# Kernel optimization log

Hardware: AMD Instinct MI355X
Metric: run time of the kernel (lower is better)

Reference implementation:

```python
import jax, jax.numpy as jnp
import numpy as np

B, C, H, W = 8, 64, 64, 64
MID = C // 8  # = 8, single-head key/query dim


def setup_inputs() -> dict:
    key = jax.random.key(0)
    ks = jax.random.split(key, 8)
    return {
        "x": jax.random.normal(ks[0], (B, C, H, W), dtype=jnp.float32),
        "wq": jax.random.normal(ks[1], (MID, C), dtype=jnp.float32) * 0.1,
        "bq": jax.random.normal(ks[2], (MID,), dtype=jnp.float32) * 0.1,
        "wk": jax.random.normal(ks[3], (MID, C), dtype=jnp.float32) * 0.1,
        "bk": jax.random.normal(ks[4], (MID,), dtype=jnp.float32) * 0.1,
        "wv": jax.random.normal(ks[5], (C, C), dtype=jnp.float32) * 0.1,
        "bv": jax.random.normal(ks[6], (C,), dtype=jnp.float32) * 0.1,
        "gamma": jax.random.uniform(ks[7], (1,), dtype=jnp.float32),
    }


def reference(x, wq, bq, wk, bk, wv, bv, gamma):
    b, c, h, w = x.shape
    n = h * w
    xf = x.reshape(b, c, n)  # [B, C, N]
    # 1x1 convs == per-pixel linear projections
    q = jnp.einsum("mc,bcn->bmn", wq, xf) + bq[:, None]  # [B, MID, N]
    k = jnp.einsum("mc,bcn->bmn", wk, xf) + bk[:, None]  # [B, MID, N]
    v = jnp.einsum("dc,bcn->bdn", wv, xf) + bv[:, None]  # [B, C, N]
    # attn[b, i, j] = softmax_j( q[:, i] . k[:, j] )  -- no scaling (SAGAN)
    attn = jax.nn.softmax(jnp.einsum("bmi,bmj->bij", q, k), axis=-1)  # [B, N, N]
    # out[b, c, i] = sum_j v[b, c, j] * attn[b, i, j]
    out = jnp.einsum("bcj,bij->bci", v, attn).reshape(b, c, h, w)
    return x + gamma[0] * out
```

## Files before the change

### kernel.cpp

```cpp
#include <hip/hip_runtime.h>
#include <math.h>

#define NB 8
#define NC 64
#define NN 4096
#define PS 72
#define LOG2E 1.4426950408889634f

typedef __attribute__((ext_vector_type(8))) short short8;
typedef __attribute__((ext_vector_type(4))) float float4v;

#if __has_builtin(__builtin_amdgcn_exp2f)
#define EXP2F(v) __builtin_amdgcn_exp2f(v)
#else
#define EXP2F(v) __expf((v) * 0.6931471805599453f)
#endif

__device__ inline unsigned short f2bf(float f) {
    unsigned int u = __builtin_bit_cast(unsigned int, f);
    unsigned int r = (u + 0x7FFFu + ((u >> 16) & 1u)) >> 16;
    return (unsigned short)r;
}
__device__ inline unsigned int bfpack(float lo, float hi) {
    unsigned int a = __builtin_bit_cast(unsigned int, lo) + 0x8000u;
    unsigned int b = __builtin_bit_cast(unsigned int, hi) + 0x8000u;
    return __builtin_amdgcn_perm(b, a, 0x07060302u);
}

__global__ __launch_bounds__(256) void prepack_kernel(
    const float* __restrict__ wq, const float* __restrict__ bq,
    const float* __restrict__ wk, const float* __restrict__ bk,
    const float* __restrict__ wv, const float* __restrict__ bv,
    unsigned short* __restrict__ wpack, float* __restrict__ bpack)
{
    const int tid = threadIdx.x;
    for (int item = tid; item < 640; item += 256) {
        const int f = item >> 6, lane = item & 63;
        const int mt = f >> 1, kc = f & 1;
        const int c0 = lane & 15, quad = lane >> 4;
        const float* row;
        float scale = 1.f;
        if (mt < 4) row = wv + (mt * 16 + c0) * 64;
        else if (c0 < 8) { row = wq + c0 * 64; scale = LOG2E; }
        else row = wk + (c0 - 8) * 64;
        unsigned short* dst = wpack + ((size_t)f * 64 + lane) * 8;
        for (int e = 0; e < 8; ++e) dst[e] = f2bf(row[kc * 32 + quad * 8 + e] * scale);
    }
    if (tid < 80) {
        float v;
        if (tid < 64) v = bv[tid];
        else if (tid < 72) v = bq[tid - 64] * LOG2E;
        else v = bk[tid - 72];
        bpack[tid] = v;
    }
}

__global__ __launch_bounds__(64) void proj_mfma_kernel(
    const float* __restrict__ x,
    const unsigned short* __restrict__ wpack, const float* __restrict__ bpack,
    unsigned short* __restrict__ qo8, unsigned short* __restrict__ ko8,
    unsigned short* __restrict__ vo)
{
    const int b = blockIdx.y;
    const int lane = threadIdx.x;
    const int c0 = lane & 15, quad = lane >> 4;
    const int n0 = blockIdx.x * 16;

    __shared__ unsigned short qkb[16][24];

    short8 wf[10];
#pragma unroll
    for (int f = 0; f < 10; ++f)
        wf[f] = *(const short8*)(wpack + ((size_t)f * 64 + lane) * 8);

    const float* xb = x + (size_t)b * NC * NN + n0 + c0;
    short8 xf[2];
#pragma unroll
    for (int kc = 0; kc < 2; ++kc)
#pragma unroll
        for (int e = 0; e < 8; ++e)
            xf[kc][e] = (short)f2bf(xb[(size_t)(kc * 32 + quad * 8 + e) * NN]);

#pragma unroll
    for (int mt = 0; mt < 4; ++mt) {
        float4v acc = {0.f, 0.f, 0.f, 0.f};
        acc = __builtin_amdgcn_mfma_f32_16x16x32_bf16(wf[mt * 2], xf[0], acc, 0, 0, 0);
        acc = __builtin_amdgcn_mfma_f32_16x16x32_bf16(wf[mt * 2 + 1], xf[1], acc, 0, 0, 0);
#pragma unroll
        for (int reg = 0; reg < 4; ++reg) {
            int ch = mt * 16 + quad * 4 + reg;
            vo[((size_t)b * NC + ch) * NN + n0 + c0] = f2bf(acc[reg] + bpack[ch]);
        }
    }

    {
        float4v acc = {0.f, 0.f, 0.f, 0.f};
        acc = __builtin_amdgcn_mfma_f32_16x16x32_bf16(wf[8], xf[0], acc, 0, 0, 0);
        acc = __builtin_amdgcn_mfma_f32_16x16x32_bf16(wf[9], xf[1], acc, 0, 0, 0);
        float a[4];
#pragma unroll
        for (int reg = 0; reg < 4; ++reg)
            a[reg] = acc[reg] + bpack[64 + quad * 4 + reg];
        *(uint2*)&qkb[c0][quad * 4] = make_uint2(bfpack(a[0], a[1]), bfpack(a[2], a[3]));
        if (quad == 0) {
            uint4 qrow = *(const uint4*)&qkb[c0][0];
            uint4 krow = *(const uint4*)&qkb[c0][8];
            *(uint4*)&qo8[((size_t)b * NN + n0 + c0) * 8] = qrow;
            *(uint4*)&ko8[((size_t)b * NN + n0 + c0) * 8] = krow;
        }
    }
}

__global__ __launch_bounds__(256, 4) void attn_fused_kernel(
    const unsigned short* __restrict__ qo8, const unsigned short* __restrict__ ko8,
    const unsigned short* __restrict__ vo,
    const float* __restrict__ x, const float* __restrict__ gamma,
    float* __restrict__ out)
{
    const int b = blockIdx.x;
    const int i0b = blockIdx.y * 32;
    const int wave = threadIdx.x >> 6, lane = threadIdx.x & 63;
    const int c0 = lane & 15, quad = lane >> 4;

    __shared__ __align__(16) float obuf[4][32][65];
    __shared__ float lbuf[4][2][16];

    unsigned short* psw = (unsigned short*)obuf + wave * 16 * PS;
    unsigned short* pswr = psw + c0 * PS + quad * 4;
    const unsigned short* psrd = psw + c0 * PS + quad * 8;

    const int jbase = wave * (NN / 4);

    short8 qf[2] = {};
    if (quad == 0) {
        qf[0] = *(const short8*)(qo8 + ((size_t)b * NN + i0b + c0) * 8);
        qf[1] = *(const short8*)(qo8 + ((size_t)b * NN + i0b + 16 + c0) * 8);
    } else if (quad == 1) {
        qf[0][0] = (short)0xC1E7;
        qf[1][0] = (short)0xC1E7;
    }

    float4v acc[2][4];
#pragma unroll
    for (int qh = 0; qh < 2; ++qh)
#pragma unroll
        for (int ct = 0; ct < 4; ++ct) acc[qh][ct] = (float4v){0.f, 0.f, 0.f, 0.f};
    float lsum[2] = {0.f, 0.f};

    const unsigned short* vbase = vo + ((size_t)b * NC + c0) * NN + jbase + quad * 8;
    const unsigned short* kbase = ko8 + ((size_t)(b * NN + jbase + c0)) * 8;

    short8 vc0[4];
#pragma unroll
    for (int ct = 0; ct < 4; ++ct)
        vc0[ct] = *(const short8*)(vbase + (size_t)ct * 16 * NN);

    for (int t = 0; t < NN / 4 / 64; ++t) {
        const int jt = t * 64;
        short8 kf[4] = {};
        if (quad == 0) {
#pragma unroll
            for (int st = 0; st < 4; ++st)
                kf[st] = *(const short8*)(kbase + (size_t)(jt + st * 16) * 8);
        } else if (quad == 1) {
            kf[0][0] = (short)0x3F80; kf[1][0] = (short)0x3F80;
            kf[2][0] = (short)0x3F80; kf[3][0] = (short)0x3F80;
        }
        short8 vc1[4], vn0[4];
#pragma unroll
        for (int ct = 0; ct < 4; ++ct)
            vc1[ct] = *(const short8*)(vbase + (size_t)ct * 16 * NN + jt + 32);
        if (t < NN / 4 / 64 - 1) {
#pragma unroll
            for (int ct = 0; ct < 4; ++ct)
                vn0[ct] = *(const short8*)(vbase + (size_t)ct * 16 * NN + jt + 64);
        }

#pragma unroll
        for (int qh = 0; qh < 2; ++qh) {
            float4v s[4];
#pragma unroll
            for (int st = 0; st < 4; ++st) {
                float4v z = {0.f, 0.f, 0.f, 0.f};
                s[st] = __builtin_amdgcn_mfma_f32_16x16x32_bf16(kf[st], qf[qh], z, 0, 0, 0);
            }
#pragma unroll
            for (int st = 0; st < 4; ++st) {
                float p0 = EXP2F(s[st][0]);
                float p1 = EXP2F(s[st][1]);
                float p2 = EXP2F(s[st][2]);
                float p3 = EXP2F(s[st][3]);
                lsum[qh] += (p0 + p1) + (p2 + p3);
                *(uint2*)(pswr + st * 16) = make_uint2(bfpack(p0, p1), bfpack(p2, p3));
            }
            {
                short8 pf0 = *(const short8*)(psrd);
#pragma unroll
                for (int ct = 0; ct < 4; ++ct)
                    acc[qh][ct] = __builtin_amdgcn_mfma_f32_16x16x32_bf16(
                        pf0, vc0[ct], acc[qh][ct], 0, 0, 0);
                short8 pf1 = *(const short8*)(psrd + 32);
#pragma unroll
                for (int ct = 0; ct < 4; ++ct)
                    acc[qh][ct] = __builtin_amdgcn_mfma_f32_16x16x32_bf16(
                        pf1, vc1[ct], acc[qh][ct], 0, 0, 0);
            }
        }
#pragma unroll
        for (int ct = 0; ct < 4; ++ct) vc0[ct] = vn0[ct];
    }

#pragma unroll
    for (int qh = 0; qh < 2; ++qh) {
        lsum[qh] += __shfl_xor(lsum[qh], 16);
        lsum[qh] += __shfl_xor(lsum[qh], 32);
    }

    __syncthreads();

    if (quad == 0) {
        lbuf[wave][0][c0] = lsum[0];
        lbuf[wave][1][c0] = lsum[1];
    }
#pragma unroll
    for (int qh = 0; qh < 2; ++qh)
#pragma unroll
        for (int ct = 0; ct < 4; ++ct)
#pragma unroll
            for (int reg = 0; reg < 4; ++reg)
                obuf[wave][qh * 16 + quad * 4 + reg][ct * 16 + c0] = acc[qh][ct][reg];
    __syncthreads();

    const int q = threadIdx.x & 31;
    const int cg = threadIdx.x >> 5;
    const float L = lbuf[0][q >> 4][q & 15] + lbuf[1][q >> 4][q & 15] +
                    lbuf[2][q >> 4][q & 15] + lbuf[3][q >> 4][q & 15];
    const float scale = gamma[0] / L;
    const size_t base = (size_t)b * NC * NN + i0b + q;
#pragma unroll
    for (int cc = 0; cc < 8; ++cc) {
        const int ch = cg * 8 + cc;
        const float O = obuf[0][q][ch] + obuf[1][q][ch] + obuf[2][q][ch] + obuf[3][q][ch];
        const size_t idx = base + (size_t)ch * NN;
        out[idx] = x[idx] + scale * O;
    }
}

extern "C" void kernel_launch(void* const* d_in, const int* in_sizes, int n_in,
                              void* d_out, int out_size, void* d_ws, size_t ws_size,
                              hipStream_t stream) {
    const float* x     = (const float*)d_in[0];
    const float* wq    = (const float*)d_in[1];
    const float* bq    = (const float*)d_in[2];
    const float* wk    = (const float*)d_in[3];
    const float* bk    = (const float*)d_in[4];
    const float* bv    = (const float*)d_in[6];
    const float* wv    = (const float*)d_in[5];
    const float* gamma = (const float*)d_in[7];
    float* out = (float*)d_out;

    float* bpack = (float*)d_ws;
    unsigned short* wpack = (unsigned short*)(bpack + 128);
    unsigned short* qo8 = wpack + 10 * 64 * 8;
    unsigned short* ko8 = qo8 + (size_t)NB * NN * 8;
    unsigned short* vo  = ko8 + (size_t)NB * NN * 8;

    prepack_kernel<<<1, 256, 0, stream>>>(wq, bq, wk, bk, wv, bv, wpack, bpack);
    proj_mfma_kernel<<<dim3(NN / 16, NB), 64, 0, stream>>>(x, wpack, bpack, qo8, ko8, vo);
    attn_fused_kernel<<<dim3(NB, NN / 32), 256, 0, stream>>>(qo8, ko8, vo, x, gamma, out);
}
```

Before: 157.2 us.

## Shrink attention LDS by packing partial outputs to bf16 and drop V prefetch

```diff
diff --git a/kernel.cpp b/kernel.cpp
--- a/kernel.cpp
+++ b/kernel.cpp
@@ -13,7 +13,7 @@
 #if __has_builtin(__builtin_amdgcn_exp2f)
 #define EXP2F(v) __builtin_amdgcn_exp2f(v)
 #else
-#define EXP2F(v) __expf((v) * 0.6931471805599453f)
+#define EXP2F(v) exp2f(v)
 #endif
 
 __device__ inline unsigned short f2bf(float f) {
@@ -92,7 +92,6 @@
             vo[((size_t)b * NC + ch) * NN + n0 + c0] = f2bf(acc[reg] + bpack[ch]);
         }
     }
-
     {
         float4v acc = {0.f, 0.f, 0.f, 0.f};
         acc = __builtin_amdgcn_mfma_f32_16x16x32_bf16(wf[8], xf[0], acc, 0, 0, 0);
@@ -122,10 +121,10 @@
     const int wave = threadIdx.x >> 6, lane = threadIdx.x & 63;
     const int c0 = lane & 15, quad = lane >> 4;
 
-    __shared__ __align__(16) float obuf[4][32][65];
+    __shared__ unsigned int obuf[4][64][17];
     __shared__ float lbuf[4][2][16];
 
-    unsigned short* psw = (unsigned short*)obuf + wave * 16 * PS;
+    unsigned short* psw = (unsigned short*)&obuf[wave][0][0];
     unsigned short* pswr = psw + c0 * PS + quad * 4;
     const unsigned short* psrd = psw + c0 * PS + quad * 8;
 
@@ -139,6 +138,8 @@
         qf[0][0] = (short)0xC1E7;
         qf[1][0] = (short)0xC1E7;
     }
+    short8 kcst = {};
+    if (quad == 1) kcst[0] = (short)0x3F80;
 
     float4v acc[2][4];
 #pragma unroll
@@ -150,31 +151,20 @@
     const unsigned short* vbase = vo + ((size_t)b * NC + c0) * NN + jbase + quad * 8;
     const unsigned short* kbase = ko8 + ((size_t)(b * NN + jbase + c0)) * 8;
 
-    short8 vc0[4];
-#pragma unroll
-    for (int ct = 0; ct < 4; ++ct)
-        vc0[ct] = *(const short8*)(vbase + (size_t)ct * 16 * NN);
-
     for (int t = 0; t < NN / 4 / 64; ++t) {
         const int jt = t * 64;
-        short8 kf[4] = {};
+        short8 kf[4] = {kcst, kcst, kcst, kcst};
         if (quad == 0) {
 #pragma unroll
             for (int st = 0; st < 4; ++st)
                 kf[st] = *(const short8*)(kbase + (size_t)(jt + st * 16) * 8);
-        } else if (quad == 1) {
-            kf[0][0] = (short)0x3F80; kf[1][0] = (short)0x3F80;
-            kf[2][0] = (short)0x3F80; kf[3][0] = (short)0x3F80;
-        }
-        short8 vc1[4], vn0[4];
+        }
+        short8 vf[4][2];
 #pragma unroll
         for (int ct = 0; ct < 4; ++ct)
-            vc1[ct] = *(const short8*)(vbase + (size_t)ct * 16 * NN + jt + 32);
-        if (t < NN / 4 / 64 - 1) {
-#pragma unroll
-            for (int ct = 0; ct < 4; ++ct)
-                vn0[ct] = *(const short8*)(vbase + (size_t)ct * 16 * NN + jt + 64);
-        }
+#pragma unroll
+            for (int kc = 0; kc < 2; ++kc)
+                vf[ct][kc] = *(const short8*)(vbase + (size_t)ct * 16 * NN + jt + kc * 32);
 
 #pragma unroll
         for (int qh = 0; qh < 2; ++qh) {
@@ -198,16 +188,14 @@
 #pragma unroll
                 for (int ct = 0; ct < 4; ++ct)
                     acc[qh][ct] = __builtin_amdgcn_mfma_f32_16x16x32_bf16(
-                        pf0, vc0[ct], acc[qh][ct], 0, 0, 0);
+                        pf0, vf[ct][0], acc[qh][ct], 0, 0, 0);
                 short8 pf1 = *(const short8*)(psrd + 32);
 #pragma unroll
                 for (int ct = 0; ct < 4; ++ct)
                     acc[qh][ct] = __builtin_amdgcn_mfma_f32_16x16x32_bf16(
-                        pf1, vc1[ct], acc[qh][ct], 0, 0, 0);
+                        pf1, vf[ct][1], acc[qh][ct], 0, 0, 0);
             }
         }
-#pragma unroll
-        for (int ct = 0; ct < 4; ++ct) vc0[ct] = vn0[ct];
     }
 
 #pragma unroll
@@ -215,20 +203,20 @@
         lsum[qh] += __shfl_xor(lsum[qh], 16);
         lsum[qh] += __shfl_xor(lsum[qh], 32);
     }
-
-    __syncthreads();
-
     if (quad == 0) {
         lbuf[wave][0][c0] = lsum[0];
         lbuf[wave][1][c0] = lsum[1];
     }
+
 #pragma unroll
     for (int qh = 0; qh < 2; ++qh)
 #pragma unroll
-        for (int ct = 0; ct < 4; ++ct)
-#pragma unroll
-            for (int reg = 0; reg < 4; ++reg)
-                obuf[wave][qh * 16 + quad * 4 + reg][ct * 16 + c0] = acc[qh][ct][reg];
+        for (int ct = 0; ct < 4; ++ct) {
+            const int ch = ct * 16 + c0;
+            *(uint2*)&obuf[wave][ch][qh * 8 + quad * 2] =
+                make_uint2(bfpack(acc[qh][ct][0], acc[qh][ct][1]),
+                           bfpack(acc[qh][ct][2], acc[qh][ct][3]));
+        }
     __syncthreads();
 
     const int q = threadIdx.x & 31;
@@ -236,11 +224,16 @@
     const float L = lbuf[0][q >> 4][q & 15] + lbuf[1][q >> 4][q & 15] +
                     lbuf[2][q >> 4][q & 15] + lbuf[3][q >> 4][q & 15];
     const float scale = gamma[0] / L;
+    const int d = ((q >> 4) << 3) | ((q & 12) >> 1) | ((q & 2) >> 1);
+    const int sh = (q & 1) << 4;
     const size_t base = (size_t)b * NC * NN + i0b + q;
 #pragma unroll
     for (int cc = 0; cc < 8; ++cc) {
         const int ch = cg * 8 + cc;
-        const float O = obuf[0][q][ch] + obuf[1][q][ch] + obuf[2][q][ch] + obuf[3][q][ch];
+        float O = 0.f;
+#pragma unroll
+        for (int w = 0; w < 4; ++w)
+            O += __builtin_bit_cast(float, (obuf[w][ch][d] >> sh) << 16);
         const size_t idx = base + (size_t)ch * NN;
         out[idx] = x[idx] + scale * O;
     }
@@ -254,8 +247,8 @@
     const float* bq    = (const float*)d_in[2];
     const float* wk    = (const float*)d_in[3];
     const float* bk    = (const float*)d_in[4];
+    const float* wv    = (const float*)d_in[5];
     const float* bv    = (const float*)d_in[6];
-    const float* wv    = (const float*)d_in[5];
     const float* gamma = (const float*)d_in[7];
     float* out = (float*)d_out;
 
```

Result: faster. 150.2 us (-4.5%).
